# Kernel tuning notes

Measured on AMD Instinct MI355X. Metric: run time of the kernel, lower is better.

The kernel has to match this reference:

```python
import jax, jax.numpy as jnp
import numpy as np

VOCAB = 32000
EMBED = 256
HID = 512
SOS_ID = 1
EOS_ID = 2
PAD_ID = 0


def setup_inputs() -> dict:
    key = jax.random.key(0)
    ks = jax.random.split(key, 8)
    B, L = 64, 49
    scale = 0.02
    return {
        "features": jax.random.normal(ks[0], (B, L, HID), jnp.float32),
        "emb": jax.random.normal(ks[1], (VOCAB, EMBED), jnp.float32) * scale,
        "W_ih": jax.random.normal(ks[2], (3 * HID, EMBED), jnp.float32) * scale,
        "W_hh": jax.random.normal(ks[3], (3 * HID, HID), jnp.float32) * scale,
        "b_ih": jax.random.normal(ks[4], (3 * HID,), jnp.float32) * scale,
        "b_hh": jax.random.normal(ks[5], (3 * HID,), jnp.float32) * scale,
        "W_out": jax.random.normal(ks[6], (VOCAB, HID), jnp.float32) * scale,
        "b_out": jax.random.normal(ks[7], (VOCAB,), jnp.float32) * scale,
        "max_len": 20,
    }


def _gru_cell(x, h, W_ih, W_hh, b_ih, b_hh):
    # torch.nn.GRUCell semantics (gates ordered r, z, n)
    gi = x @ W_ih.T + b_ih  # [B, 3H]
    gh = h @ W_hh.T + b_hh  # [B, 3H]
    i_r, i_z, i_n = jnp.split(gi, 3, axis=-1)
    h_r, h_z, h_n = jnp.split(gh, 3, axis=-1)
    r = jax.nn.sigmoid(i_r + h_r)
    z = jax.nn.sigmoid(i_z + h_z)
    n = jnp.tanh(i_n + r * h_n)
    return (1.0 - z) * n + z * h


def reference(features, emb, W_ih, W_hh, b_ih, b_hh, W_out, b_out, max_len):
    B = features.shape[0]
    h0 = features.mean(axis=1)  # [B, HID]
    x0 = emb[jnp.full((B,), SOS_ID, dtype=jnp.int32)]  # [B, EMBED]
    done0 = jnp.zeros((B,), dtype=bool)

    def step(carry, _):
        h, x, done = carry
        h = _gru_cell(x, h, W_ih, W_hh, b_ih, b_hh)
        logits = h @ W_out.T + b_out  # [B, VOCAB]
        pred = jnp.argmax(logits, axis=-1)  # [B]
        is_eos = pred == EOS_ID
        # original appends word only if sequence not complete and token != <EOS>
        tok = jnp.where(done | is_eos, PAD_ID, pred)
        done = done | is_eos
        x = emb[pred]  # greedy feedback
        return (h, x, done), (logits, tok)

    _, (logits, toks) = jax.lax.scan(step, (h0, x0, done0), None, length=max_len)
    # [T, B, V] -> [B, T, V]; [T, B] -> [B, T]
    return toks.T, jnp.transpose(logits, (1, 0, 2))
```

## Files before the change

kernel.cpp:

```cpp
#include <hip/hip_runtime.h>
#include <stdint.h>

#define VOCABN 32000
#define EMBEDN 256
#define HIDN   512
#define BN     64
#define SOSID  1
#define EOSID  2
#define NSUB   8

typedef __attribute__((ext_vector_type(8))) short short8;
typedef __attribute__((ext_vector_type(4))) float f32x4;

__device__ __forceinline__ unsigned ordf(float f) {
  unsigned u = __float_as_uint(f);
  return (u & 0x80000000u) ? ~u : (u | 0x80000000u);
}
__device__ __forceinline__ int decode_pred(unsigned long long pk) {
  return (int)(0xFFFFFFFFu - (unsigned)(pk & 0xFFFFFFFFull));
}
__device__ __forceinline__ unsigned short f2bf(float x) {
  unsigned u = __float_as_uint(x);
  unsigned r = (u + 0x7FFFu + ((u >> 16) & 1u)) >> 16;
  return (unsigned short)r;
}
__device__ __forceinline__ float bf2f(unsigned short h) {
  return __uint_as_float(((unsigned)h) << 16);
}
__device__ __forceinline__ f32x4 mfma3(short8 ah, short8 al, short8 bh, short8 bl,
                                       f32x4 acc) {
  acc = __builtin_amdgcn_mfma_f32_16x16x32_bf16(ah, bh, acc, 0, 0, 0);
  acc = __builtin_amdgcn_mfma_f32_16x16x32_bf16(ah, bl, acc, 0, 0, 0);
  acc = __builtin_amdgcn_mfma_f32_16x16x32_bf16(al, bh, acc, 0, 0, 0);
  return acc;
}

__global__ void k_init(const float* __restrict__ feat, float* __restrict__ h0,
                       int L, int* __restrict__ done, char* __restrict__ Hsp0) {
  int b = blockIdx.x, tid = threadIdx.x;
  float inv = 1.0f / (float)L;
  for (int j = tid; j < HIDN; j += 256) {
    const float* p = feat + (size_t)b * L * HIDN + j;
    float s = 0.f;
    for (int l = 0; l < L; ++l) s += p[(size_t)l * HIDN];
    float hv = s * inv;
    h0[b * HIDN + j] = hv;
    unsigned short hi = f2bf(hv);
    unsigned short lo = f2bf(hv - bf2f(hi));
    int bt = b >> 4, col = b & 15, kt = j >> 5, kr = j & 31;
    int ln = ((kr >> 3) << 4) | col, e = kr & 7;
    size_t off = (size_t)(bt * 16 + kt) * 2048 + ln * 16 + e * 2;
    *(unsigned short*)(Hsp0 + off) = hi;
    *(unsigned short*)(Hsp0 + off + 1024) = lo;
  }
  if (b == 0 && tid < 2 * BN) done[tid] = 0;
}

__global__ __launch_bounds__(256) void k_splitW(const float* __restrict__ W,
                                                char* __restrict__ Wsp,
                                                int ktshift, int K) {
  int tid = threadIdx.x, lane = tid & 63, tl = tid >> 6;
  int tile = blockIdx.x * 4 + tl;
  int vt = tile >> ktshift, kt = tile & ((1 << ktshift) - 1);
  int v = vt * 16 + (lane & 15);
  int k0 = kt * 32 + ((lane >> 4) << 3);
  const float* src = W + (size_t)v * K + k0;
  float xv[8];
  *(float4*)&xv[0] = *(const float4*)src;
  *(float4*)&xv[4] = *(const float4*)(src + 4);
  unsigned short h[8], l[8];
  #pragma unroll
  for (int i = 0; i < 8; ++i) {
    h[i] = f2bf(xv[i]);
    l[i] = f2bf(xv[i] - bf2f(h[i]));
  }
  uint4 H, Lw;
  H.x = (unsigned)h[0] | ((unsigned)h[1] << 16);
  H.y = (unsigned)h[2] | ((unsigned)h[3] << 16);
  H.z = (unsigned)h[4] | ((unsigned)h[5] << 16);
  H.w = (unsigned)h[6] | ((unsigned)h[7] << 16);
  Lw.x = (unsigned)l[0] | ((unsigned)l[1] << 16);
  Lw.y = (unsigned)l[2] | ((unsigned)l[3] << 16);
  Lw.z = (unsigned)l[4] | ((unsigned)l[5] << 16);
  Lw.w = (unsigned)l[6] | ((unsigned)l[7] << 16);
  char* dst = Wsp + (size_t)tile * 2048 + lane * 16;
  *(uint4*)dst = H;
  *(uint4*)(dst + 1024) = Lw;
}

__global__ __launch_bounds__(256) void k_gh(
    const float* __restrict__ emb, const char* __restrict__ Wihsp,
    const char* __restrict__ Whhsp, const float* __restrict__ b_ih,
    const float* __restrict__ b_hh, const float* __restrict__ h_rd,
    float* __restrict__ h_wr, const char* __restrict__ Hsp_rd,
    char* __restrict__ Hsp_wr,
    const unsigned long long* __restrict__ s_rd,
    unsigned long long* __restrict__ s_wr,
    const int* __restrict__ done_rd, int* __restrict__ done_wr,
    float* __restrict__ out_toks, int t, int T) {
  __shared__ int preds[16];
  __shared__ float red[3][4][256];
  int tid = threadIdx.x, lane = tid & 63, wid = tid >> 6;
  int jt = blockIdx.x >> 2, bt = blockIdx.x & 3;

  if (tid < 16) {
    int pr = SOSID;
    if (t) {
      unsigned long long mx = 0ull;
      #pragma unroll
      for (int s = 0; s < NSUB; ++s) {
        unsigned long long v = s_rd[s * BN + bt * 16 + tid];
        mx = (v > mx) ? v : mx;
      }
      pr = decode_pred(mx);
    }
    preds[tid] = pr;
  }
  if (blockIdx.x == 0) {
    s_wr[tid] = 0ull;
    s_wr[256 + tid] = 0ull;
    if (t >= 1 && tid < BN) {
      unsigned long long mx = 0ull;
      #pragma unroll
      for (int s = 0; s < NSUB; ++s) {
        unsigned long long v = s_rd[s * BN + tid];
        mx = (v > mx) ? v : mx;
      }
      int pred = decode_pred(mx);
      int iseos = (pred == EOSID) ? 1 : 0;
      int dold = done_rd[tid];
      out_toks[(size_t)tid * T + (t - 1)] = (float)((dold | iseos) ? 0 : pred);
      done_wr[tid] = dold | iseos;
    }
  }
  __syncthreads();

  int col = lane & 15, rg = lane >> 4;
  int xrow = preds[col];
  f32x4 acc_r = {0.f, 0.f, 0.f, 0.f}, acc_z = {0.f, 0.f, 0.f, 0.f};
  f32x4 acc_gin = {0.f, 0.f, 0.f, 0.f}, acc_ghn = {0.f, 0.f, 0.f, 0.f};

  #pragma unroll
  for (int u = 0; u < 6; ++u) {
    int g = wid * 6 + u;
    if (g < 8) {
      float xv[8];
      const float* src = emb + (size_t)xrow * EMBEDN + g * 32 + rg * 8;
      *(float4*)&xv[0] = *(const float4*)src;
      *(float4*)&xv[4] = *(const float4*)(src + 4);
      unsigned short hi[8], lo[8];
      #pragma unroll
      for (int i = 0; i < 8; ++i) {
        hi[i] = f2bf(xv[i]);
        lo[i] = f2bf(xv[i] - bf2f(hi[i]));
      }
      short8 xh, xl;
      #pragma unroll
      for (int i = 0; i < 8; ++i) { xh[i] = (short)hi[i]; xl[i] = (short)lo[i]; }
      const char* pr_ = Wihsp + (size_t)((jt) * 8 + g) * 2048 + lane * 16;
      const char* pz_ = Wihsp + (size_t)((32 + jt) * 8 + g) * 2048 + lane * 16;
      const char* pn_ = Wihsp + (size_t)((64 + jt) * 8 + g) * 2048 + lane * 16;
      acc_r = mfma3(*(const short8*)pr_, *(const short8*)(pr_ + 1024), xh, xl, acc_r);
      acc_z = mfma3(*(const short8*)pz_, *(const short8*)(pz_ + 1024), xh, xl, acc_z);
      acc_gin = mfma3(*(const short8*)pn_, *(const short8*)(pn_ + 1024), xh, xl, acc_gin);
    } else {
      int kt = g - 8;
      const char* bq = Hsp_rd + (size_t)(bt * 16 + kt) * 2048 + lane * 16;
      short8 hh = *(const short8*)bq;
      short8 hl = *(const short8*)(bq + 1024);
      const char* pr_ = Whhsp + (size_t)((jt) * 16 + kt) * 2048 + lane * 16;
      const char* pz_ = Whhsp + (size_t)((32 + jt) * 16 + kt) * 2048 + lane * 16;
      const char* pn_ = Whhsp + (size_t)((64 + jt) * 16 + kt) * 2048 + lane * 16;
      acc_r = mfma3(*(const short8*)pr_, *(const short8*)(pr_ + 1024), hh, hl, acc_r);
      acc_z = mfma3(*(const short8*)pz_, *(const short8*)(pz_ + 1024), hh, hl, acc_z);
      acc_ghn = mfma3(*(const short8*)pn_, *(const short8*)(pn_ + 1024), hh, hl, acc_ghn);
    }
  }

  if (wid) {
    *(f32x4*)&red[wid - 1][0][lane * 4] = acc_r;
    *(f32x4*)&red[wid - 1][1][lane * 4] = acc_z;
    *(f32x4*)&red[wid - 1][2][lane * 4] = acc_gin;
    *(f32x4*)&red[wid - 1][3][lane * 4] = acc_ghn;
  }
  __syncthreads();
  if (wid == 0) {
    #pragma unroll
    for (int w = 0; w < 3; ++w) {
      acc_r += *(f32x4*)&red[w][0][lane * 4];
      acc_z += *(f32x4*)&red[w][1][lane * 4];
      acc_gin += *(f32x4*)&red[w][2][lane * 4];
      acc_ghn += *(f32x4*)&red[w][3][lane * 4];
    }
    int j0 = jt * 16, j = j0 + rg * 4;
    int b = bt * 16 + col;
    float4 bir = *(const float4*)(b_ih + j);
    float4 bhr = *(const float4*)(b_hh + j);
    float4 biz = *(const float4*)(b_ih + 512 + j);
    float4 bhz = *(const float4*)(b_hh + 512 + j);
    float4 bin = *(const float4*)(b_ih + 1024 + j);
    float4 bhn = *(const float4*)(b_hh + 1024 + j);
    float bra[4] = {bir.x + bhr.x, bir.y + bhr.y, bir.z + bhr.z, bir.w + bhr.w};
    float bza[4] = {biz.x + bhz.x, biz.y + bhz.y, biz.z + bhz.z, biz.w + bhz.w};
    float bia[4] = {bin.x, bin.y, bin.z, bin.w};
    float bha[4] = {bhn.x, bhn.y, bhn.z, bhn.w};
    float4 hold = *(const float4*)(h_rd + (size_t)b * HIDN + j);
    float ho[4] = {hold.x, hold.y, hold.z, hold.w};
    float hn[4];
    unsigned short hi[4], lo[4];
    #pragma unroll
    for (int reg = 0; reg < 4; ++reg) {
      float r = 1.f / (1.f + expf(-(acc_r[reg] + bra[reg])));
      float z = 1.f / (1.f + expf(-(acc_z[reg] + bza[reg])));
      float n = tanhf(acc_gin[reg] + bia[reg] + r * (acc_ghn[reg] + bha[reg]));
      hn[reg] = (1.f - z) * n + z * ho[reg];
      hi[reg] = f2bf(hn[reg]);
      lo[reg] = f2bf(hn[reg] - bf2f(hi[reg]));
    }
    float4 hout = {hn[0], hn[1], hn[2], hn[3]};
    *(float4*)(h_wr + (size_t)b * HIDN + j) = hout;
    int kt2 = j >> 5, kr2 = j & 31;
    int ln2 = ((kr2 >> 3) << 4) | col, e2 = kr2 & 7;
    char* dst = Hsp_wr + ((size_t)((b >> 4) * 16 + kt2) * 2048 + ln2 * 16 + e2 * 2);
    uint2 Hp, Lp;
    Hp.x = (unsigned)hi[0] | ((unsigned)hi[1] << 16);
    Hp.y = (unsigned)hi[2] | ((unsigned)hi[3] << 16);
    Lp.x = (unsigned)lo[0] | ((unsigned)lo[1] << 16);
    Lp.y = (unsigned)lo[2] | ((unsigned)lo[3] << 16);
    *(uint2*)dst = Hp;
    *(uint2*)(dst + 1024) = Lp;
  }
}

__global__ __launch_bounds__(256) void k_logits4(
    const char* __restrict__ Wsp, const char* __restrict__ Hsp,
    const float* __restrict__ bout, float* __restrict__ out_logits,
    unsigned long long* __restrict__ slots, int t, int T) {
  __shared__ f32x4 red[3][8][64];
  int tid = threadIdx.x, lane = tid & 63, wid = tid >> 6;
  int v0 = blockIdx.x * 32, vt = v0 >> 4;
  int sub = blockIdx.x & (NSUB - 1);

  f32x4 acc[4][2];
  #pragma unroll
  for (int nb = 0; nb < 4; ++nb)
    #pragma unroll
    for (int mv = 0; mv < 2; ++mv)
      acc[nb][mv] = (f32x4){0.f, 0.f, 0.f, 0.f};

  #pragma unroll 2
  for (int kk = 0; kk < 4; ++kk) {
    int kt = wid * 4 + kk;
    short8 ah[4], al[4], wh[2], wl[2];
    #pragma unroll
    for (int nb = 0; nb < 4; ++nb) {
      const char* q = Hsp + (size_t)(nb * 16 + kt) * 2048 + lane * 16;
      ah[nb] = *(const short8*)q;
      al[nb] = *(const short8*)(q + 1024);
    }
    #pragma unroll
    for (int mv = 0; mv < 2; ++mv) {
      const char* p = Wsp + (size_t)((vt + mv) * 16 + kt) * 2048 + lane * 16;
      wh[mv] = *(const short8*)p;
      wl[mv] = *(const short8*)(p + 1024);
    }
    #pragma unroll
    for (int nb = 0; nb < 4; ++nb)
      #pragma unroll
      for (int mv = 0; mv < 2; ++mv)
        acc[nb][mv] = mfma3(ah[nb], al[nb], wh[mv], wl[mv], acc[nb][mv]);
  }

  if (wid) {
    #pragma unroll
    for (int nb = 0; nb < 4; ++nb)
      #pragma unroll
      for (int mv = 0; mv < 2; ++mv)
        red[wid - 1][nb * 2 + mv][lane] = acc[nb][mv];
  }
  __syncthreads();
  if (wid == 0) {
    #pragma unroll
    for (int w = 0; w < 3; ++w)
      #pragma unroll
      for (int nb = 0; nb < 4; ++nb)
        #pragma unroll
        for (int mv = 0; mv < 2; ++mv)
          acc[nb][mv] += red[w][nb * 2 + mv][lane];

    int col = lane & 15, rg = lane >> 4;
    float bvv[2] = {bout[v0 + col], bout[v0 + 16 + col]};
    unsigned long long key[4][4];
    #pragma unroll
    for (int nb = 0; nb < 4; ++nb)
      #pragma unroll
      for (int reg = 0; reg < 4; ++reg) key[nb][reg] = 0ull;

    #pragma unroll
    for (int nb = 0; nb < 4; ++nb) {
      #pragma unroll
      for (int mv = 0; mv < 2; ++mv) {
        int v = v0 + mv * 16 + col;
        #pragma unroll
        for (int reg = 0; reg < 4; ++reg) {
          float val = acc[nb][mv][reg] + bvv[mv];
          int b = nb * 16 + rg * 4 + reg;
          __builtin_nontemporal_store(
              val, out_logits + ((size_t)b * T + t) * VOCABN + v);
          unsigned long long pk = ((unsigned long long)ordf(val) << 32) |
                                  (unsigned long long)(0xFFFFFFFFu - (unsigned)v);
          key[nb][reg] = (pk > key[nb][reg]) ? pk : key[nb][reg];
        }
      }
    }
    #pragma unroll
    for (int m = 1; m < 16; m <<= 1) {
      #pragma unroll
      for (int nb = 0; nb < 4; ++nb)
        #pragma unroll
        for (int reg = 0; reg < 4; ++reg) {
          unsigned long long o = __shfl_xor(key[nb][reg], m, 64);
          key[nb][reg] = (o > key[nb][reg]) ? o : key[nb][reg];
        }
    }
    if (col == 0) {
      #pragma unroll
      for (int nb = 0; nb < 4; ++nb)
        #pragma unroll
        for (int reg = 0; reg < 4; ++reg) {
          int b = nb * 16 + rg * 4 + reg;
          atomicMax(slots + sub * BN + b, key[nb][reg]);
        }
    }
  }
}

__global__ void k_final(const unsigned long long* __restrict__ slots,
                        const int* __restrict__ done_rd,
                        float* __restrict__ out_toks, int T) {
  int b = threadIdx.x;
  if (b < BN) {
    unsigned long long mx = 0ull;
    #pragma unroll
    for (int s = 0; s < NSUB; ++s) {
      unsigned long long v = slots[s * BN + b];
      mx = (v > mx) ? v : mx;
    }
    int pred = decode_pred(mx);
    int iseos = (pred == EOSID) ? 1 : 0;
    int tok = (done_rd[b] || iseos) ? 0 : pred;
    out_toks[(size_t)b * T + (T - 1)] = (float)tok;
  }
}

extern "C" void kernel_launch(void* const* d_in, const int* in_sizes, int n_in,
                              void* d_out, int out_size, void* d_ws, size_t ws_size,
                              hipStream_t stream) {
  const float* feat = (const float*)d_in[0];
  const float* emb  = (const float*)d_in[1];
  const float* W_ih = (const float*)d_in[2];
  const float* W_hh = (const float*)d_in[3];
  const float* b_ih = (const float*)d_in[4];
  const float* b_hh = (const float*)d_in[5];
  const float* Wout = (const float*)d_in[6];
  const float* bout = (const float*)d_in[7];

  int L = in_sizes[0] / (BN * HIDN);
  int T = out_size / (BN * (VOCABN + 1));
  if (T <= 0) T = 20;

  float* out_toks   = (float*)d_out;
  float* out_logits = (float*)d_out + (size_t)BN * T;

  char* w = (char*)d_ws;
  float* hbuf = (float*)w;  w += (size_t)2 * BN * HIDN * sizeof(float);
  int*   done = (int*)w;    w += (size_t)2 * BN * sizeof(int);
  w = (char*)(((uintptr_t)w + 511) & ~(uintptr_t)511);
  unsigned long long* slots2 = (unsigned long long*)w;
  w += (size_t)2 * NSUB * BN * sizeof(unsigned long long);
  w = (char*)(((uintptr_t)w + 511) & ~(uintptr_t)511);
  char* Hsp   = w;          w += (size_t)2 * 4 * 16 * 2048;
  char* Wihsp = w;          w += (size_t)96 * 8 * 2048;
  char* Whhsp = w;          w += (size_t)96 * 16 * 2048;
  char* Wsp   = w;          w += (size_t)2000 * 16 * 2048;

  k_init<<<BN, 256, 0, stream>>>(feat, hbuf, L, done, Hsp);
  k_splitW<<<2000 * 16 / 4, 256, 0, stream>>>(Wout, Wsp, 4, 512);
  k_splitW<<<96 * 8 / 4, 256, 0, stream>>>(W_ih, Wihsp, 3, 256);
  k_splitW<<<96 * 16 / 4, 256, 0, stream>>>(W_hh, Whhsp, 4, 512);

  for (int t = 0; t < T; ++t) {
    const float* h_rd = hbuf + (size_t)(t & 1) * BN * HIDN;
    float* h_wr       = hbuf + (size_t)((t + 1) & 1) * BN * HIDN;
    const char* Hsp_rd = Hsp + (size_t)(t & 1) * 131072;
    char* Hsp_wr       = Hsp + (size_t)((t + 1) & 1) * 131072;
    const unsigned long long* s_rd = slots2 + ((t + 1) & 1) * NSUB * BN;
    unsigned long long* s_wr       = slots2 + (t & 1) * NSUB * BN;
    const int* drd = done + (t & 1) * BN;
    int* dwr       = done + ((t + 1) & 1) * BN;

    k_gh<<<128, 256, 0, stream>>>(emb, Wihsp, Whhsp, b_ih, b_hh, h_rd, h_wr,
                                  Hsp_rd, Hsp_wr, s_rd, s_wr, drd, dwr,
                                  out_toks, t, T);
    k_logits4<<<VOCABN / 32, 256, 0, stream>>>(Wsp, Hsp_wr, bout, out_logits,
                                               s_wr, t, T);
  }
  k_final<<<1, 64, 0, stream>>>(slots2 + ((T - 1) & 1) * NSUB * BN,
                                done + (T & 1) * BN, out_toks, T);
}
```

Before: 636.7 us.

## Widen GRU gate kernel to 8 waves and stage W_out tiles via LDS

The GRU gate kernel now runs 512 threads: each of 8 waves handles one input-embedding k-tile and two hidden k-tiles, and the cross-wave reduction grows to 7 partials. This spreads the serial per-wave MFMA chain across more waves. The logits kernel first copies its 64KB block of split W_out tiles into LDS with global_load_lds, then reads the MFMA operands from LDS, and its k-loop is fully unrolled. The staging adds a barrier and 64KB of LDS per block, which cuts occupancy and does not reuse the weights across waves, so it may add latency rather than hide it.

```diff
diff --git a/kernel.cpp b/kernel.cpp
--- a/kernel.cpp
+++ b/kernel.cpp
@@ -33,6 +33,15 @@
   acc = __builtin_amdgcn_mfma_f32_16x16x32_bf16(ah, bl, acc, 0, 0, 0);
   acc = __builtin_amdgcn_mfma_f32_16x16x32_bf16(al, bh, acc, 0, 0, 0);
   return acc;
+}
+__device__ __forceinline__ void stage16(const char* g, char* lds_uniform, int lane) {
+#if __has_builtin(__builtin_amdgcn_global_load_lds)
+  __builtin_amdgcn_global_load_lds(
+      (const __attribute__((address_space(1))) char*)(g + lane * 16),
+      (__attribute__((address_space(3))) char*)lds_uniform, 16, 0, 0);
+#else
+  *(uint4*)(lds_uniform + lane * 16) = *(const uint4*)(g + lane * 16);
+#endif
 }
 
 __global__ void k_init(const float* __restrict__ feat, float* __restrict__ h0,
@@ -88,7 +97,7 @@
   *(uint4*)(dst + 1024) = Lw;
 }
 
-__global__ __launch_bounds__(256) void k_gh(
+__global__ __launch_bounds__(512) void k_gh2(
     const float* __restrict__ emb, const char* __restrict__ Wihsp,
     const char* __restrict__ Whhsp, const float* __restrict__ b_ih,
     const float* __restrict__ b_hh, const float* __restrict__ h_rd,
@@ -99,7 +108,7 @@
     const int* __restrict__ done_rd, int* __restrict__ done_wr,
     float* __restrict__ out_toks, int t, int T) {
   __shared__ int preds[16];
-  __shared__ float red[3][4][256];
+  __shared__ __align__(16) float red[7][4][256];
   int tid = threadIdx.x, lane = tid & 63, wid = tid >> 6;
   int jt = blockIdx.x >> 2, bt = blockIdx.x & 3;
 
@@ -118,7 +127,6 @@
   }
   if (blockIdx.x == 0) {
     s_wr[tid] = 0ull;
-    s_wr[256 + tid] = 0ull;
     if (t >= 1 && tid < BN) {
       unsigned long long mx = 0ull;
       #pragma unroll
@@ -138,59 +146,56 @@
   int col = lane & 15, rg = lane >> 4;
   int xrow = preds[col];
   f32x4 acc_r = {0.f, 0.f, 0.f, 0.f}, acc_z = {0.f, 0.f, 0.f, 0.f};
-  f32x4 acc_gin = {0.f, 0.f, 0.f, 0.f}, acc_ghn = {0.f, 0.f, 0.f, 0.f};
-
+  f32x4 acc_nx = {0.f, 0.f, 0.f, 0.f}, acc_nh = {0.f, 0.f, 0.f, 0.f};
+
+  {
+    int xu = wid;
+    float xv[8];
+    const float* src = emb + (size_t)xrow * EMBEDN + xu * 32 + rg * 8;
+    *(float4*)&xv[0] = *(const float4*)src;
+    *(float4*)&xv[4] = *(const float4*)(src + 4);
+    short8 xh, xl;
+    #pragma unroll
+    for (int i = 0; i < 8; ++i) {
+      unsigned short h = f2bf(xv[i]);
+      xh[i] = (short)h;
+      xl[i] = (short)f2bf(xv[i] - bf2f(h));
+    }
+    const char* p0 = Wihsp + (size_t)((0 * 32 + jt) * 8 + xu) * 2048 + lane * 16;
+    const char* p1 = Wihsp + (size_t)((1 * 32 + jt) * 8 + xu) * 2048 + lane * 16;
+    const char* p2 = Wihsp + (size_t)((2 * 32 + jt) * 8 + xu) * 2048 + lane * 16;
+    acc_r  = mfma3(*(const short8*)p0, *(const short8*)(p0 + 1024), xh, xl, acc_r);
+    acc_z  = mfma3(*(const short8*)p1, *(const short8*)(p1 + 1024), xh, xl, acc_z);
+    acc_nx = mfma3(*(const short8*)p2, *(const short8*)(p2 + 1024), xh, xl, acc_nx);
+  }
   #pragma unroll
-  for (int u = 0; u < 6; ++u) {
-    int g = wid * 6 + u;
-    if (g < 8) {
-      float xv[8];
-      const float* src = emb + (size_t)xrow * EMBEDN + g * 32 + rg * 8;
-      *(float4*)&xv[0] = *(const float4*)src;
-      *(float4*)&xv[4] = *(const float4*)(src + 4);
-      unsigned short hi[8], lo[8];
-      #pragma unroll
-      for (int i = 0; i < 8; ++i) {
-        hi[i] = f2bf(xv[i]);
-        lo[i] = f2bf(xv[i] - bf2f(hi[i]));
-      }
-      short8 xh, xl;
-      #pragma unroll
-      for (int i = 0; i < 8; ++i) { xh[i] = (short)hi[i]; xl[i] = (short)lo[i]; }
-      const char* pr_ = Wihsp + (size_t)((jt) * 8 + g) * 2048 + lane * 16;
-      const char* pz_ = Wihsp + (size_t)((32 + jt) * 8 + g) * 2048 + lane * 16;
-      const char* pn_ = Wihsp + (size_t)((64 + jt) * 8 + g) * 2048 + lane * 16;
-      acc_r = mfma3(*(const short8*)pr_, *(const short8*)(pr_ + 1024), xh, xl, acc_r);
-      acc_z = mfma3(*(const short8*)pz_, *(const short8*)(pz_ + 1024), xh, xl, acc_z);
-      acc_gin = mfma3(*(const short8*)pn_, *(const short8*)(pn_ + 1024), xh, xl, acc_gin);
-    } else {
-      int kt = g - 8;
-      const char* bq = Hsp_rd + (size_t)(bt * 16 + kt) * 2048 + lane * 16;
-      short8 hh = *(const short8*)bq;
-      short8 hl = *(const short8*)(bq + 1024);
-      const char* pr_ = Whhsp + (size_t)((jt) * 16 + kt) * 2048 + lane * 16;
-      const char* pz_ = Whhsp + (size_t)((32 + jt) * 16 + kt) * 2048 + lane * 16;
-      const char* pn_ = Whhsp + (size_t)((64 + jt) * 16 + kt) * 2048 + lane * 16;
-      acc_r = mfma3(*(const short8*)pr_, *(const short8*)(pr_ + 1024), hh, hl, acc_r);
-      acc_z = mfma3(*(const short8*)pz_, *(const short8*)(pz_ + 1024), hh, hl, acc_z);
-      acc_ghn = mfma3(*(const short8*)pn_, *(const short8*)(pn_ + 1024), hh, hl, acc_ghn);
-    }
+  for (int q = 0; q < 2; ++q) {
+    int hu = wid * 2 + q;
+    const char* bq = Hsp_rd + (size_t)(bt * 16 + hu) * 2048 + lane * 16;
+    short8 hh = *(const short8*)bq;
+    short8 hl = *(const short8*)(bq + 1024);
+    const char* p0 = Whhsp + (size_t)((0 * 32 + jt) * 16 + hu) * 2048 + lane * 16;
+    const char* p1 = Whhsp + (size_t)((1 * 32 + jt) * 16 + hu) * 2048 + lane * 16;
+    const char* p2 = Whhsp + (size_t)((2 * 32 + jt) * 16 + hu) * 2048 + lane * 16;
+    acc_r  = mfma3(*(const short8*)p0, *(const short8*)(p0 + 1024), hh, hl, acc_r);
+    acc_z  = mfma3(*(const short8*)p1, *(const short8*)(p1 + 1024), hh, hl, acc_z);
+    acc_nh = mfma3(*(const short8*)p2, *(const short8*)(p2 + 1024), hh, hl, acc_nh);
   }
 
   if (wid) {
     *(f32x4*)&red[wid - 1][0][lane * 4] = acc_r;
     *(f32x4*)&red[wid - 1][1][lane * 4] = acc_z;
-    *(f32x4*)&red[wid - 1][2][lane * 4] = acc_gin;
-    *(f32x4*)&red[wid - 1][3][lane * 4] = acc_ghn;
+    *(f32x4*)&red[wid - 1][2][lane * 4] = acc_nx;
+    *(f32x4*)&red[wid - 1][3][lane * 4] = acc_nh;
   }
   __syncthreads();
   if (wid == 0) {
     #pragma unroll
-    for (int w = 0; w < 3; ++w) {
-      acc_r += *(f32x4*)&red[w][0][lane * 4];
-      acc_z += *(f32x4*)&red[w][1][lane * 4];
-      acc_gin += *(f32x4*)&red[w][2][lane * 4];
-      acc_ghn += *(f32x4*)&red[w][3][lane * 4];
+    for (int w = 0; w < 7; ++w) {
+      acc_r  += *(f32x4*)&red[w][0][lane * 4];
+      acc_z  += *(f32x4*)&red[w][1][lane * 4];
+      acc_nx += *(f32x4*)&red[w][2][lane * 4];
+      acc_nh += *(f32x4*)&red[w][3][lane * 4];
     }
     int j0 = jt * 16, j = j0 + rg * 4;
     int b = bt * 16 + col;
@@ -212,7 +217,7 @@
     for (int reg = 0; reg < 4; ++reg) {
       float r = 1.f / (1.f + expf(-(acc_r[reg] + bra[reg])));
       float z = 1.f / (1.f + expf(-(acc_z[reg] + bza[reg])));
-      float n = tanhf(acc_gin[reg] + bia[reg] + r * (acc_ghn[reg] + bha[reg]));
+      float n = tanhf(acc_nx[reg] + bia[reg] + r * (acc_nh[reg] + bha[reg]));
       hn[reg] = (1.f - z) * n + z * ho[reg];
       hi[reg] = f2bf(hn[reg]);
       lo[reg] = f2bf(hn[reg] - bf2f(hi[reg]));
@@ -232,15 +237,26 @@
   }
 }
 
-__global__ __launch_bounds__(256) void k_logits4(
+__global__ __launch_bounds__(256) void k_logits5(
     const char* __restrict__ Wsp, const char* __restrict__ Hsp,
     const float* __restrict__ bout, float* __restrict__ out_logits,
     unsigned long long* __restrict__ slots, int t, int T) {
+  __shared__ __align__(16) char ldsW[32 * 2048];
   __shared__ f32x4 red[3][8][64];
   int tid = threadIdx.x, lane = tid & 63, wid = tid >> 6;
   int v0 = blockIdx.x * 32, vt = v0 >> 4;
   int sub = blockIdx.x & (NSUB - 1);
 
+  #pragma unroll
+  for (int i = 0; i < 16; ++i) {
+    int u = wid * 16 + i;
+    int tile = u >> 1, half = u & 1;
+    int mv = tile >> 4, kt = tile & 15;
+    const char* src = Wsp + (size_t)((vt + mv) * 16 + kt) * 2048 + half * 1024;
+    stage16(src, ldsW + tile * 2048 + half * 1024, lane);
+  }
+  __syncthreads();
+
   f32x4 acc[4][2];
   #pragma unroll
   for (int nb = 0; nb < 4; ++nb)
@@ -248,7 +264,7 @@
     for (int mv = 0; mv < 2; ++mv)
       acc[nb][mv] = (f32x4){0.f, 0.f, 0.f, 0.f};
 
-  #pragma unroll 2
+  #pragma unroll
   for (int kk = 0; kk < 4; ++kk) {
     int kt = wid * 4 + kk;
     short8 ah[4], al[4], wh[2], wl[2];
@@ -260,7 +276,7 @@
     }
     #pragma unroll
     for (int mv = 0; mv < 2; ++mv) {
-      const char* p = Wsp + (size_t)((vt + mv) * 16 + kt) * 2048 + lane * 16;
+      const char* p = ldsW + (mv * 16 + kt) * 2048 + lane * 16;
       wh[mv] = *(const short8*)p;
       wl[mv] = *(const short8*)(p + 1024);
     }
@@ -399,10 +415,10 @@
     const int* drd = done + (t & 1) * BN;
     int* dwr       = done + ((t + 1) & 1) * BN;
 
-    k_gh<<<128, 256, 0, stream>>>(emb, Wihsp, Whhsp, b_ih, b_hh, h_rd, h_wr,
-                                  Hsp_rd, Hsp_wr, s_rd, s_wr, drd, dwr,
-                                  out_toks, t, T);
-    k_logits4<<<VOCABN / 32, 256, 0, stream>>>(Wsp, Hsp_wr, bout, out_logits,
+    k_gh2<<<128, 512, 0, stream>>>(emb, Wihsp, Whhsp, b_ih, b_hh, h_rd, h_wr,
+                                   Hsp_rd, Hsp_wr, s_rd, s_wr, drd, dwr,
+                                   out_toks, t, T);
+    k_logits5<<<VOCABN / 32, 256, 0, stream>>>(Wsp, Hsp_wr, bout, out_logits,
                                                s_wr, t, T);
   }
   k_final<<<1, 64, 0, stream>>>(slots2 + ((T - 1) & 1) * NSUB * BN,
```

Measured after the change: 921.6 us. +44.7%, slower.
